# Kernel optimization log

Hardware: AMD Instinct MI355X
Metric: run time of the kernel (lower is better)

## Reference

```python
import jax, jax.numpy as jnp
import numpy as np

N_BLOCKS = 16
BLOCK_SIZE = 512
TOP_K = N_BLOCKS // 4  # matches n_blocks // 4 in the source


def setup_inputs() -> dict:
    key = jax.random.key(0)
    k1, k2, k3, k4, k5 = jax.random.split(key, 5)
    in_f, out_f = 2048, 8192
    x = jax.random.normal(k1, (2, 4096, in_f), dtype=jnp.float32)
    # router: Linear(in_features, n_blocks)
    Wr = jax.random.normal(k2, (N_BLOCKS, in_f), dtype=jnp.float32) * (in_f ** -0.5)
    br = jnp.zeros((N_BLOCKS,), dtype=jnp.float32)
    # fc1: Linear(in, out); fc2: Linear(out, in). Biases are unused in the original forward.
    W1 = jax.random.normal(k3, (out_f, in_f), dtype=jnp.float32) * (in_f ** -0.5)
    W2 = jax.random.normal(k4, (in_f, out_f), dtype=jnp.float32) * (out_f ** -0.5)
    return {"x": x, "Wr": Wr, "br": br, "W1": W1, "W2": W2}


def reference(x, Wr, br, W1, W2):
    x_shape = x.shape
    in_f = x_shape[-1]
    xf = x.reshape(-1, in_f)                      # [N, in]
    n = xf.shape[0]
    # router + top-k block selection per token
    prob = jax.nn.softmax(xf @ Wr.T + br, axis=-1)          # [N, nb]
    _, idx = jax.lax.top_k(prob, TOP_K)                      # [N, k]
    mask = jnp.zeros((n, N_BLOCKS), dtype=xf.dtype)
    mask = mask.at[jnp.arange(n)[:, None], idx].set(1.0)     # [N, nb]
    # fc1 per block: h[n,i,b] = x @ W1_block_i^T  (bias never used in source)
    W1b = W1.reshape(N_BLOCKS, BLOCK_SIZE, in_f)
    h = jnp.einsum('nf,ibf->nib', xf, W1b)                   # [N, nb, bs]
    # activation, then zero out unselected blocks (unselected never reach fc2)
    h = jax.nn.gelu(h, approximate=False) * mask[:, :, None]
    # fc2 per block accumulate: y = sum_i h_i @ W2_block_i^T
    W2b = W2.reshape(in_f, N_BLOCKS, BLOCK_SIZE)
    y = jnp.einsum('nib,fib->nf', h, W2b)                    # [N, in]
    return y.reshape(x_shape)
```

## Files before the change

kernel.cpp:

```cpp
#include <hip/hip_runtime.h>
#include <hip/hip_bf16.h>

#define N_TOK 8192
#define IN_F  2048
#define OUT_F 8192
#define NB    16
#define BS    512
#define BM    128
#define MAX_MT 272

typedef short          bf16x8  __attribute__((ext_vector_type(8)));
typedef unsigned short ushort8 __attribute__((ext_vector_type(8)));
typedef float          f32x4   __attribute__((ext_vector_type(4)));
typedef _Float16       f16x8   __attribute__((ext_vector_type(8)));

#define WS_COUNTS 0
#define WS_TSTART 64
#define WS_SEL    256
#define WS_INV    (32*1024)
#define WS_LISTS  (192*1024)
#define WS_XBF    (1ull<<20)
#define WS_W1BF   (WS_XBF + 33554432ull)
#define WS_W2BF   WS_XBF
#define WS_H      (WS_XBF + 67108864ull)
#define WS_YP     (WS_H + 35651584ull)

static __device__ __forceinline__ unsigned short f2bf(float f) {
    __hip_bfloat16 h = __float2bfloat16(f);
    return *reinterpret_cast<unsigned short*>(&h);
}

static __device__ __forceinline__ void gload16(const unsigned short* g, unsigned short* lds) {
    __builtin_amdgcn_global_load_lds(
        (const __attribute__((address_space(1))) unsigned int*)g,
        (__attribute__((address_space(3))) unsigned int*)lds, 16, 0, 0);
}

#define MFMA16(ai, bi) \
    acc[0][0] = __builtin_amdgcn_mfma_f32_16x16x32_bf16(ai##0, bi##0, acc[0][0], 0, 0, 0); \
    acc[0][1] = __builtin_amdgcn_mfma_f32_16x16x32_bf16(ai##0, bi##1, acc[0][1], 0, 0, 0); \
    acc[0][2] = __builtin_amdgcn_mfma_f32_16x16x32_bf16(ai##0, bi##2, acc[0][2], 0, 0, 0); \
    acc[0][3] = __builtin_amdgcn_mfma_f32_16x16x32_bf16(ai##0, bi##3, acc[0][3], 0, 0, 0); \
    acc[1][0] = __builtin_amdgcn_mfma_f32_16x16x32_bf16(ai##1, bi##0, acc[1][0], 0, 0, 0); \
    acc[1][1] = __builtin_amdgcn_mfma_f32_16x16x32_bf16(ai##1, bi##1, acc[1][1], 0, 0, 0); \
    acc[1][2] = __builtin_amdgcn_mfma_f32_16x16x32_bf16(ai##1, bi##2, acc[1][2], 0, 0, 0); \
    acc[1][3] = __builtin_amdgcn_mfma_f32_16x16x32_bf16(ai##1, bi##3, acc[1][3], 0, 0, 0); \
    acc[2][0] = __builtin_amdgcn_mfma_f32_16x16x32_bf16(ai##2, bi##0, acc[2][0], 0, 0, 0); \
    acc[2][1] = __builtin_amdgcn_mfma_f32_16x16x32_bf16(ai##2, bi##1, acc[2][1], 0, 0, 0); \
    acc[2][2] = __builtin_amdgcn_mfma_f32_16x16x32_bf16(ai##2, bi##2, acc[2][2], 0, 0, 0); \
    acc[2][3] = __builtin_amdgcn_mfma_f32_16x16x32_bf16(ai##2, bi##3, acc[2][3], 0, 0, 0); \
    acc[3][0] = __builtin_amdgcn_mfma_f32_16x16x32_bf16(ai##3, bi##0, acc[3][0], 0, 0, 0); \
    acc[3][1] = __builtin_amdgcn_mfma_f32_16x16x32_bf16(ai##3, bi##1, acc[3][1], 0, 0, 0); \
    acc[3][2] = __builtin_amdgcn_mfma_f32_16x16x32_bf16(ai##3, bi##2, acc[3][2], 0, 0, 0); \
    acc[3][3] = __builtin_amdgcn_mfma_f32_16x16x32_bf16(ai##3, bi##3, acc[3][3], 0, 0, 0);

__global__ __launch_bounds__(256) void router_kernel(
    const float* __restrict__ x, const float* __restrict__ Wr,
    const float* __restrict__ br, unsigned short* __restrict__ sel)
{
    const int tid = threadIdx.x;
    const int lt = tid & 63;
    const int wv = tid >> 6;
    const int tok = blockIdx.x * 4 + wv;
    const int e = lt >> 2, p = lt & 3;
    const float4* xp = (const float4*)(x + (size_t)tok * IN_F);
    const float4* wp = (const float4*)(Wr + (size_t)e * IN_F);
    double s = 0.0;
    for (int j = p; j < IN_F / 4; j += 4) {
        float4 a = xp[j], w = wp[j];
        s += (double)a.x * w.x + (double)a.y * w.y + (double)a.z * w.z + (double)a.w * w.w;
    }
    s += __shfl_down(s, 2);
    s += __shfl_down(s, 1);
    __shared__ double logits[4][NB];
    if (p == 0) logits[wv][e] = s + (double)br[e];
    __syncthreads();
    if (lt == 0) {
        unsigned used = 0, packed = 0;
        #pragma unroll
        for (int kk = 0; kk < 4; ++kk) {
            int best = 0; double bv = -1.0e300;
            #pragma unroll
            for (int i = 0; i < NB; ++i)
                if (!((used >> i) & 1u) && logits[wv][i] > bv) { bv = logits[wv][i]; best = i; }
            used |= 1u << best;
            packed |= (unsigned)best << (4 * kk);
        }
        sel[tok] = (unsigned short)packed;
    }
}

__global__ __launch_bounds__(256) void build_lists_kernel(
    const unsigned short* __restrict__ sel, int* __restrict__ counts,
    int* __restrict__ lists, unsigned* __restrict__ inv)
{
    const int e = blockIdx.x;
    const int t = threadIdx.x;
    unsigned short mysel[N_TOK / 256];
    int cnt = 0;
    #pragma unroll
    for (int i = 0; i < N_TOK / 256; ++i) {
        unsigned s = sel[i * 256 + t];
        mysel[i] = (unsigned short)s;
        bool m = ((s & 15u) == (unsigned)e) | (((s >> 4) & 15u) == (unsigned)e) |
                 (((s >> 8) & 15u) == (unsigned)e) | (((s >> 12) & 15u) == (unsigned)e);
        cnt += m ? 1 : 0;
    }
    __shared__ int ps[256];
    ps[t] = cnt;
    __syncthreads();
    #pragma unroll
    for (int off = 1; off < 256; off <<= 1) {
        int v = (t >= off) ? ps[t - off] : 0;
        __syncthreads();
        ps[t] += v;
        __syncthreads();
    }
    int pos = ps[t] - cnt;
    if (t == 255) counts[e] = ps[255];
    #pragma unroll
    for (int i = 0; i < N_TOK / 256; ++i) {
        unsigned s = mysel[i];
        bool m = ((s & 15u) == (unsigned)e) | (((s >> 4) & 15u) == (unsigned)e) |
                 (((s >> 8) & 15u) == (unsigned)e) | (((s >> 12) & 15u) == (unsigned)e);
        if (m) {
            const int tok = i * 256 + t;
            int j = ((s & 15u) == (unsigned)e) ? 0 :
                    (((s >> 4) & 15u) == (unsigned)e) ? 1 :
                    (((s >> 8) & 15u) == (unsigned)e) ? 2 : 3;
            inv[tok * 4 + j] = ((unsigned)e << 16) | (unsigned)pos;
            lists[e * N_TOK + pos++] = tok;
        }
    }
}

__global__ void scan_kernel(const int* __restrict__ counts, int* __restrict__ tstart)
{
    if (threadIdx.x == 0) {
        int acc = 0;
        for (int i = 0; i < NB; ++i) { tstart[i] = acc; acc += (counts[i] + BM - 1) / BM; }
        tstart[NB] = acc;
    }
}

__global__ __launch_bounds__(256) void convert_swz_kernel(
    const float* __restrict__ src, unsigned short* __restrict__ dst, int sh)
{
    const int total = 1 << 21;
    for (int id = blockIdx.x * 256 + threadIdx.x; id < total; id += 2048 * 256) {
        const int row = id >> sh;
        const int sr  = id & ((1 << sh) - 1);
        const int ps  = sr ^ (row & 7);
        const float4* s4 = (const float4*)(src + ((size_t)id << 3));
        float4 p0 = s4[0], p1 = s4[1];
        ushort8 o;
        o[0] = f2bf(p0.x); o[1] = f2bf(p0.y); o[2] = f2bf(p0.z); o[3] = f2bf(p0.w);
        o[4] = f2bf(p1.x); o[5] = f2bf(p1.y); o[6] = f2bf(p1.z); o[7] = f2bf(p1.w);
        *(ushort8*)(dst + (((size_t)(row) << sh) << 3) + ((size_t)ps << 3)) = o;
    }
}

__global__ __launch_bounds__(256) void fc1_kernel(
    const unsigned short* __restrict__ x_bf, const unsigned short* __restrict__ w1_bf,
    const int* __restrict__ lists, const int* __restrict__ counts,
    const int* __restrict__ tstart, unsigned short* __restrict__ h)
{
    __shared__ unsigned short As[2][BM * 64];
    __shared__ unsigned short Bs[2][BM * 64];
    const int bid = blockIdx.x;
    const int newid = (bid & 7) * 136 + (bid >> 3);
    const int nt = newid & 3, mt = newid >> 2;
    if (mt >= tstart[NB]) return;
    int b = 0;
    #pragma unroll
    for (int i = 1; i < NB; ++i) b += (mt >= tstart[i]);
    const int cnt  = counts[b];
    const int row0 = (mt - tstart[b]) * BM;
    const int tid  = threadIdx.x;
    const int wave = tid >> 6, lane = tid & 63;
    const int sr8 = lane >> 3, sph = lane & 7;

    const unsigned short* aS[4];
    const unsigned short* bS[4];
    const int loff = wave * 2048;
    #pragma unroll
    for (int t = 0; t < 4; ++t) {
        const int r = wave * 32 + t * 8 + sr8;
        const int gr = min(row0 + r, cnt - 1);
        const int tok = lists[b * N_TOK + gr];
        aS[t] = x_bf + (size_t)tok * IN_F + ((sph ^ sr8 ^ (tok & 7)) << 3);
        bS[t] = w1_bf + (size_t)(b * BS + nt * BM + r) * IN_F + (sph << 3);
    }

    const int lr16 = lane & 15, q = lane >> 4;
    const int wm = (wave >> 1) * 64, wn = (wave & 1) * 64;
    int offA[4], offB[4];
    #pragma unroll
    for (int i = 0; i < 4; ++i) {
        const int r = wm + i * 16 + lr16;
        offA[i] = r * 64 + ((q ^ (r & 7)) << 3);
    }
    #pragma unroll
    for (int j = 0; j < 4; ++j) {
        const int r = wn + j * 16 + lr16;
        offB[j] = r * 64 + ((q ^ (r & 7)) << 3);
    }

    f32x4 acc[4][4];
    #pragma unroll
    for (int i = 0; i < 4; ++i)
        #pragma unroll
        for (int j = 0; j < 4; ++j) acc[i][j] = (f32x4)0.0f;

    #pragma unroll
    for (int t = 0; t < 4; ++t) {
        gload16(aS[t], &As[0][loff + t * 512]);
        gload16(bS[t], &Bs[0][loff + t * 512]);
    }

    const int NK = IN_F / 64;
    for (int k = 0; k < NK; ++k) {
        const int cur = k & 1;
        if (k + 1 < NK) {
            const int ko = (k + 1) * 64;
            #pragma unroll
            for (int t = 0; t < 4; ++t) {
                gload16(aS[t] + ko, &As[cur ^ 1][loff + t * 512]);
                gload16(bS[t] + ko, &Bs[cur ^ 1][loff + t * 512]);
            }
            asm volatile("s_waitcnt vmcnt(8)" ::: "memory");
        } else {
            asm volatile("s_waitcnt vmcnt(0)" ::: "memory");
        }
        __builtin_amdgcn_s_barrier();
        __builtin_amdgcn_sched_barrier(0);
        {
            bf16x8 a0, a1, a2, a3, b0, b1, b2, b3;
            #pragma unroll
            for (int kk = 0; kk < 2; ++kk) {
                const int kx = kk << 5;
                a0 = *(const bf16x8*)&As[cur][offA[0] ^ kx];
                a1 = *(const bf16x8*)&As[cur][offA[1] ^ kx];
                a2 = *(const bf16x8*)&As[cur][offA[2] ^ kx];
                a3 = *(const bf16x8*)&As[cur][offA[3] ^ kx];
                b0 = *(const bf16x8*)&Bs[cur][offB[0] ^ kx];
                b1 = *(const bf16x8*)&Bs[cur][offB[1] ^ kx];
                b2 = *(const bf16x8*)&Bs[cur][offB[2] ^ kx];
                b3 = *(const bf16x8*)&Bs[cur][offB[3] ^ kx];
                __builtin_amdgcn_s_setprio(1);
                MFMA16(a, b)
                __builtin_amdgcn_s_setprio(0);
            }
        }
        __builtin_amdgcn_sched_barrier(0);
        __builtin_amdgcn_s_barrier();
    }
    #pragma unroll
    for (int i = 0; i < 4; ++i) {
        #pragma unroll
        for (int r = 0; r < 4; ++r) {
            const int lrow = wm + i * 16 + q * 4 + r;
            if (row0 + lrow < cnt) {
                const size_t hrow = (size_t)(mt * BM + lrow) * BS;
                const int r7 = (lrow & 7) << 3;
                #pragma unroll
                for (int j = 0; j < 4; ++j) {
                    const int col = nt * BM + wn + j * 16 + lr16;
                    float v = acc[i][j][r];
                    v = 0.5f * v * (1.0f + erff(v * 0.70710678118654752f));
                    h[hrow + (col ^ r7)] = f2bf(v);
                }
            }
        }
    }
}

__global__ __launch_bounds__(256) void fc2_kernel(
    const unsigned short* __restrict__ h, const unsigned short* __restrict__ w2_bf,
    const int* __restrict__ counts, const int* __restrict__ tstart,
    _Float16* __restrict__ yp)
{
    __shared__ unsigned short As[2][BM * 64];
    __shared__ unsigned short Bs[2][BM * 64];
    const int bid = blockIdx.x;
    const int newid = (bid & 7) * 544 + (bid >> 3);
    const int nt = newid & 15, mt = newid >> 4;
    if (mt >= tstart[NB]) return;
    int b = 0;
    #pragma unroll
    for (int i = 1; i < NB; ++i) b += (mt >= tstart[i]);
    const int cnt  = counts[b];
    const int row0 = (mt - tstart[b]) * BM;
    const int tid  = threadIdx.x;
    const int wave = tid >> 6, lane = tid & 63;
    const int sr8 = lane >> 3, sph = lane & 7;

    const unsigned short* aS[4];
    const unsigned short* bS[4];
    const int loff = wave * 2048;
    #pragma unroll
    for (int t = 0; t < 4; ++t) {
        const int r = wave * 32 + t * 8 + sr8;
        aS[t] = h + (size_t)(mt * BM + r) * BS + (sph << 3);
        bS[t] = w2_bf + (size_t)(nt * BM + r) * OUT_F + b * BS + (sph << 3);
    }

    const int lr16 = lane & 15, q = lane >> 4;
    const int wm = (wave >> 1) * 64, wn = (wave & 1) * 64;
    int offA[4], offB[4];
    #pragma unroll
    for (int i = 0; i < 4; ++i) {
        const int r = wm + i * 16 + lr16;
        offA[i] = r * 64 + ((q ^ (r & 7)) << 3);
    }
    #pragma unroll
    for (int j = 0; j < 4; ++j) {
        const int r = wn + j * 16 + lr16;
        offB[j] = r * 64 + ((q ^ (r & 7)) << 3);
    }

    f32x4 acc[4][4];
    #pragma unroll
    for (int i = 0; i < 4; ++i)
        #pragma unroll
        for (int j = 0; j < 4; ++j) acc[i][j] = (f32x4)0.0f;

    #pragma unroll
    for (int t = 0; t < 4; ++t) {
        gload16(aS[t], &As[0][loff + t * 512]);
        gload16(bS[t], &Bs[0][loff + t * 512]);
    }

    const int NK = BS / 64;
    for (int k = 0; k < NK; ++k) {
        const int cur = k & 1;
        if (k + 1 < NK) {
            const int ko = (k + 1) * 64;
            #pragma unroll
            for (int t = 0; t < 4; ++t) {
                gload16(aS[t] + ko, &As[cur ^ 1][loff + t * 512]);
                gload16(bS[t] + ko, &Bs[cur ^ 1][loff + t * 512]);
            }
            asm volatile("s_waitcnt vmcnt(8)" ::: "memory");
        } else {
            asm volatile("s_waitcnt vmcnt(0)" ::: "memory");
        }
        __builtin_amdgcn_s_barrier();
        __builtin_amdgcn_sched_barrier(0);
        {
            bf16x8 a0, a1, a2, a3, b0, b1, b2, b3;
            #pragma unroll
            for (int kk = 0; kk < 2; ++kk) {
                const int kx = kk << 5;
                a0 = *(const bf16x8*)&As[cur][offA[0] ^ kx];
                a1 = *(const bf16x8*)&As[cur][offA[1] ^ kx];
                a2 = *(const bf16x8*)&As[cur][offA[2] ^ kx];
                a3 = *(const bf16x8*)&As[cur][offA[3] ^ kx];
                b0 = *(const bf16x8*)&Bs[cur][offB[0] ^ kx];
                b1 = *(const bf16x8*)&Bs[cur][offB[1] ^ kx];
                b2 = *(const bf16x8*)&Bs[cur][offB[2] ^ kx];
                b3 = *(const bf16x8*)&Bs[cur][offB[3] ^ kx];
                __builtin_amdgcn_s_setprio(1);
                MFMA16(a, b)
                __builtin_amdgcn_s_setprio(0);
            }
        }
        __builtin_amdgcn_sched_barrier(0);
        __builtin_amdgcn_s_barrier();
    }
    #pragma unroll
    for (int i = 0; i < 4; ++i) {
        #pragma unroll
        for (int r = 0; r < 4; ++r) {
            const int lrow = wm + i * 16 + q * 4 + r;
            if (row0 + lrow < cnt) {
                _Float16* yrow = yp + (size_t)(mt * BM + lrow) * IN_F + nt * BM + wn + lr16;
                #pragma unroll
                for (int j = 0; j < 4; ++j)
                    yrow[j * 16] = (_Float16)acc[i][j][r];
            }
        }
    }
}

__global__ __launch_bounds__(256) void reduce_kernel(
    const _Float16* __restrict__ yp, const unsigned* __restrict__ inv,
    const int* __restrict__ tstart, float* __restrict__ y)
{
    const int tok = blockIdx.x;
    __shared__ size_t rbase[4];
    if (threadIdx.x < 4) {
        unsigned v = inv[tok * 4 + threadIdx.x];
        rbase[threadIdx.x] = (size_t)(tstart[v >> 16] * BM + (int)(v & 0xFFFFu)) * IN_F;
    }
    __syncthreads();
    const int c = threadIdx.x * 8;
    f16x8 v0 = *(const f16x8*)(yp + rbase[0] + c);
    f16x8 v1 = *(const f16x8*)(yp + rbase[1] + c);
    f16x8 v2 = *(const f16x8*)(yp + rbase[2] + c);
    f16x8 v3 = *(const f16x8*)(yp + rbase[3] + c);
    float out[8];
    #pragma unroll
    for (int j = 0; j < 8; ++j)
        out[j] = (float)v0[j] + (float)v1[j] + (float)v2[j] + (float)v3[j];
    float4* yo = (float4*)(y + (size_t)tok * IN_F + c);
    yo[0] = make_float4(out[0], out[1], out[2], out[3]);
    yo[1] = make_float4(out[4], out[5], out[6], out[7]);
}

extern "C" void kernel_launch(void* const* d_in, const int* in_sizes, int n_in,
                              void* d_out, int out_size, void* d_ws, size_t ws_size,
                              hipStream_t stream) {
    const float* x  = (const float*)d_in[0];
    const float* Wr = (const float*)d_in[1];
    const float* br = (const float*)d_in[2];
    const float* W1 = (const float*)d_in[3];
    const float* W2 = (const float*)d_in[4];
    float* y = (float*)d_out;
    char* ws = (char*)d_ws;
    int* counts = (int*)(ws + WS_COUNTS);
    int* tstart = (int*)(ws + WS_TSTART);
    unsigned short* sel = (unsigned short*)(ws + WS_SEL);
    unsigned* inv = (unsigned*)(ws + WS_INV);
    int* lists  = (int*)(ws + WS_LISTS);
    unsigned short* x_bf  = (unsigned short*)(ws + WS_XBF);
    unsigned short* w1_bf = (unsigned short*)(ws + WS_W1BF);
    unsigned short* w2_bf = (unsigned short*)(ws + WS_W2BF);
    unsigned short* h     = (unsigned short*)(ws + WS_H);
    _Float16* yp          = (_Float16*)(ws + WS_YP);

    hipLaunchKernelGGL(router_kernel, dim3(N_TOK / 4), dim3(256), 0, stream, x, Wr, br, sel);
    hipLaunchKernelGGL(build_lists_kernel, dim3(NB), dim3(256), 0, stream, sel, counts, lists, inv);
    hipLaunchKernelGGL(scan_kernel, dim3(1), dim3(64), 0, stream, counts, tstart);
    hipLaunchKernelGGL(convert_swz_kernel, dim3(2048), dim3(256), 0, stream, x,  x_bf,  8);
    hipLaunchKernelGGL(convert_swz_kernel, dim3(2048), dim3(256), 0, stream, W1, w1_bf, 8);
    hipLaunchKernelGGL(fc1_kernel, dim3(4 * MAX_MT), dim3(256), 0, stream, x_bf, w1_bf, lists, counts, tstart, h);
    hipLaunchKernelGGL(convert_swz_kernel, dim3(2048), dim3(256), 0, stream, W2, w2_bf, 10);
    hipLaunchKernelGGL(fc2_kernel, dim3(16 * MAX_MT), dim3(256), 0, stream, h, w2_bf, counts, tstart, yp);
    hipLaunchKernelGGL(reduce_kernel, dim3(N_TOK), dim3(256), 0, stream, yp, inv, tstart, y);
}
```

Baseline: 430.4 us.

## Enlarge expert GEMM tiles to 256 rows with 8 waves and triple-buffered LDS

```diff
diff --git a/kernel.cpp b/kernel.cpp
--- a/kernel.cpp
+++ b/kernel.cpp
@@ -6,8 +6,8 @@
 #define OUT_F 8192
 #define NB    16
 #define BS    512
-#define BM    128
-#define MAX_MT 272
+#define BM2   256
+#define MAX_MT2 144
 
 typedef short          bf16x8  __attribute__((ext_vector_type(8)));
 typedef unsigned short ushort8 __attribute__((ext_vector_type(8)));
@@ -20,10 +20,10 @@
 #define WS_INV    (32*1024)
 #define WS_LISTS  (192*1024)
 #define WS_XBF    (1ull<<20)
-#define WS_W1BF   (WS_XBF + 33554432ull)
 #define WS_W2BF   WS_XBF
-#define WS_H      (WS_XBF + 67108864ull)
-#define WS_YP     (WS_H + 35651584ull)
+#define WS_H      (WS_XBF + 33554432ull)
+#define WS_W1BF   (WS_H + 37748736ull)
+#define WS_YP     WS_W1BF
 
 static __device__ __forceinline__ unsigned short f2bf(float f) {
     __hip_bfloat16 h = __float2bfloat16(f);
@@ -54,6 +54,16 @@
     acc[3][2] = __builtin_amdgcn_mfma_f32_16x16x32_bf16(ai##3, bi##2, acc[3][2], 0, 0, 0); \
     acc[3][3] = __builtin_amdgcn_mfma_f32_16x16x32_bf16(ai##3, bi##3, acc[3][3], 0, 0, 0);
 
+#define PHASE_TAIL \
+    __builtin_amdgcn_s_barrier(); \
+    asm volatile("s_waitcnt lgkmcnt(0)" ::: "memory"); \
+    __builtin_amdgcn_sched_barrier(0); \
+    __builtin_amdgcn_s_setprio(1); \
+    MFMA16(a, b) \
+    __builtin_amdgcn_s_setprio(0); \
+    __builtin_amdgcn_sched_barrier(0); \
+    __builtin_amdgcn_s_barrier();
+
 __global__ __launch_bounds__(256) void router_kernel(
     const float* __restrict__ x, const float* __restrict__ Wr,
     const float* __restrict__ br, unsigned short* __restrict__ sel)
@@ -138,7 +148,7 @@
 {
     if (threadIdx.x == 0) {
         int acc = 0;
-        for (int i = 0; i < NB; ++i) { tstart[i] = acc; acc += (counts[i] + BM - 1) / BM; }
+        for (int i = 0; i < NB; ++i) { tstart[i] = acc; acc += (counts[i] + BM2 - 1) / BM2; }
         tstart[NB] = acc;
     }
 }
@@ -160,51 +170,49 @@
     }
 }
 
-__global__ __launch_bounds__(256) void fc1_kernel(
+__global__ __launch_bounds__(512) void fc1_kernel(
     const unsigned short* __restrict__ x_bf, const unsigned short* __restrict__ w1_bf,
     const int* __restrict__ lists, const int* __restrict__ counts,
     const int* __restrict__ tstart, unsigned short* __restrict__ h)
 {
-    __shared__ unsigned short As[2][BM * 64];
-    __shared__ unsigned short Bs[2][BM * 64];
+    __shared__ unsigned short lds[73728];
     const int bid = blockIdx.x;
-    const int newid = (bid & 7) * 136 + (bid >> 3);
+    const int newid = (bid & 7) * 72 + (bid >> 3);
     const int nt = newid & 3, mt = newid >> 2;
     if (mt >= tstart[NB]) return;
     int b = 0;
     #pragma unroll
     for (int i = 1; i < NB; ++i) b += (mt >= tstart[i]);
     const int cnt  = counts[b];
-    const int row0 = (mt - tstart[b]) * BM;
+    const int row0 = (mt - tstart[b]) * BM2;
     const int tid  = threadIdx.x;
     const int wave = tid >> 6, lane = tid & 63;
-    const int sr8 = lane >> 3, sph = lane & 7;
+    const int sph = lane & 7;
+    const int rbase = wave * 8 + (lane >> 3);
 
     const unsigned short* aS[4];
-    const unsigned short* bS[4];
-    const int loff = wave * 2048;
-    #pragma unroll
-    for (int t = 0; t < 4; ++t) {
-        const int r = wave * 32 + t * 8 + sr8;
+    const unsigned short* bS[2];
+    #pragma unroll
+    for (int i = 0; i < 4; ++i) {
+        const int r = i * 64 + rbase;
         const int gr = min(row0 + r, cnt - 1);
         const int tok = lists[b * N_TOK + gr];
-        aS[t] = x_bf + (size_t)tok * IN_F + ((sph ^ sr8 ^ (tok & 7)) << 3);
-        bS[t] = w1_bf + (size_t)(b * BS + nt * BM + r) * IN_F + (sph << 3);
-    }
+        aS[i] = x_bf + (size_t)tok * IN_F + ((sph ^ (r & 7) ^ (tok & 7)) << 3);
+    }
+    #pragma unroll
+    for (int j = 0; j < 2; ++j) {
+        const int r = j * 64 + rbase;
+        bS[j] = w1_bf + (size_t)(b * BS + nt * 128 + r) * IN_F + (sph << 3);
+    }
+    const int wbase = wave * 512;
 
     const int lr16 = lane & 15, q = lane >> 4;
     const int wm = (wave >> 1) * 64, wn = (wave & 1) * 64;
     int offA[4], offB[4];
     #pragma unroll
-    for (int i = 0; i < 4; ++i) {
-        const int r = wm + i * 16 + lr16;
-        offA[i] = r * 64 + ((q ^ (r & 7)) << 3);
-    }
-    #pragma unroll
-    for (int j = 0; j < 4; ++j) {
-        const int r = wn + j * 16 + lr16;
-        offB[j] = r * 64 + ((q ^ (r & 7)) << 3);
-    }
+    for (int i = 0; i < 4; ++i) { const int r = wm + i * 16 + lr16; offA[i] = r * 64 + ((q ^ (r & 7)) << 3); }
+    #pragma unroll
+    for (int j = 0; j < 4; ++j) { const int r = wn + j * 16 + lr16; offB[j] = r * 64 + ((q ^ (r & 7)) << 3); }
 
     f32x4 acc[4][4];
     #pragma unroll
@@ -212,48 +220,46 @@
         #pragma unroll
         for (int j = 0; j < 4; ++j) acc[i][j] = (f32x4)0.0f;
 
-    #pragma unroll
-    for (int t = 0; t < 4; ++t) {
-        gload16(aS[t], &As[0][loff + t * 512]);
-        gload16(bS[t], &Bs[0][loff + t * 512]);
-    }
+#define STA1(k, buf, i) gload16(aS[i] + (size_t)(k) * 64, lds + (buf) * 24576 + (i) * 4096 + wbase)
+#define STB1(k, buf, j) gload16(bS[j] + (size_t)(k) * 64, lds + (buf) * 24576 + 16384 + (j) * 4096 + wbase)
+
+    STA1(0,0,0); STA1(0,0,1); STA1(0,0,2); STA1(0,0,3); STB1(0,0,0); STB1(0,0,1);
+    STA1(1,1,0); STA1(1,1,1); STA1(1,1,2); STA1(1,1,3); STB1(1,1,0); STB1(1,1,1);
+    asm volatile("s_waitcnt vmcnt(6)" ::: "memory");
+    __builtin_amdgcn_s_barrier();
 
     const int NK = IN_F / 64;
+    int cur = 0;
     for (int k = 0; k < NK; ++k) {
-        const int cur = k & 1;
-        if (k + 1 < NK) {
-            const int ko = (k + 1) * 64;
-            #pragma unroll
-            for (int t = 0; t < 4; ++t) {
-                gload16(aS[t] + ko, &As[cur ^ 1][loff + t * 512]);
-                gload16(bS[t] + ko, &Bs[cur ^ 1][loff + t * 512]);
-            }
-            asm volatile("s_waitcnt vmcnt(8)" ::: "memory");
-        } else {
+        const unsigned short* Ab = lds + cur * 24576;
+        const unsigned short* Bb = Ab + 16384;
+        const int nxt = (cur == 0) ? 2 : cur - 1;
+        bf16x8 a0 = *(const bf16x8*)&Ab[offA[0]];
+        bf16x8 a1 = *(const bf16x8*)&Ab[offA[1]];
+        bf16x8 a2 = *(const bf16x8*)&Ab[offA[2]];
+        bf16x8 a3 = *(const bf16x8*)&Ab[offA[3]];
+        bf16x8 b0 = *(const bf16x8*)&Bb[offB[0]];
+        bf16x8 b1 = *(const bf16x8*)&Bb[offB[1]];
+        bf16x8 b2 = *(const bf16x8*)&Bb[offB[2]];
+        bf16x8 b3 = *(const bf16x8*)&Bb[offB[3]];
+        if (k + 2 < NK) { STA1(k + 2, nxt, 0); STA1(k + 2, nxt, 1); STB1(k + 2, nxt, 0); }
+        PHASE_TAIL
+        a0 = *(const bf16x8*)&Ab[offA[0] ^ 32];
+        a1 = *(const bf16x8*)&Ab[offA[1] ^ 32];
+        a2 = *(const bf16x8*)&Ab[offA[2] ^ 32];
+        a3 = *(const bf16x8*)&Ab[offA[3] ^ 32];
+        b0 = *(const bf16x8*)&Bb[offB[0] ^ 32];
+        b1 = *(const bf16x8*)&Bb[offB[1] ^ 32];
+        b2 = *(const bf16x8*)&Bb[offB[2] ^ 32];
+        b3 = *(const bf16x8*)&Bb[offB[3] ^ 32];
+        if (k + 2 < NK) {
+            STA1(k + 2, nxt, 2); STA1(k + 2, nxt, 3); STB1(k + 2, nxt, 1);
+            asm volatile("s_waitcnt vmcnt(6)" ::: "memory");
+        } else if (k + 1 < NK) {
             asm volatile("s_waitcnt vmcnt(0)" ::: "memory");
         }
-        __builtin_amdgcn_s_barrier();
-        __builtin_amdgcn_sched_barrier(0);
-        {
-            bf16x8 a0, a1, a2, a3, b0, b1, b2, b3;
-            #pragma unroll
-            for (int kk = 0; kk < 2; ++kk) {
-                const int kx = kk << 5;
-                a0 = *(const bf16x8*)&As[cur][offA[0] ^ kx];
-                a1 = *(const bf16x8*)&As[cur][offA[1] ^ kx];
-                a2 = *(const bf16x8*)&As[cur][offA[2] ^ kx];
-                a3 = *(const bf16x8*)&As[cur][offA[3] ^ kx];
-                b0 = *(const bf16x8*)&Bs[cur][offB[0] ^ kx];
-                b1 = *(const bf16x8*)&Bs[cur][offB[1] ^ kx];
-                b2 = *(const bf16x8*)&Bs[cur][offB[2] ^ kx];
-                b3 = *(const bf16x8*)&Bs[cur][offB[3] ^ kx];
-                __builtin_amdgcn_s_setprio(1);
-                MFMA16(a, b)
-                __builtin_amdgcn_s_setprio(0);
-            }
-        }
-        __builtin_amdgcn_sched_barrier(0);
-        __builtin_amdgcn_s_barrier();
+        PHASE_TAIL
+        cur = (cur == 2) ? 0 : cur + 1;
     }
     #pragma unroll
     for (int i = 0; i < 4; ++i) {
@@ -261,11 +267,11 @@
         for (int r = 0; r < 4; ++r) {
             const int lrow = wm + i * 16 + q * 4 + r;
             if (row0 + lrow < cnt) {
-                const size_t hrow = (size_t)(mt * BM + lrow) * BS;
+                const size_t hrow = (size_t)(mt * BM2 + lrow) * BS;
                 const int r7 = (lrow & 7) << 3;
                 #pragma unroll
                 for (int j = 0; j < 4; ++j) {
-                    const int col = nt * BM + wn + j * 16 + lr16;
+                    const int col = nt * 128 + wn + j * 16 + lr16;
                     float v = acc[i][j][r];
                     v = 0.5f * v * (1.0f + erff(v * 0.70710678118654752f));
                     h[hrow + (col ^ r7)] = f2bf(v);
@@ -273,51 +279,51 @@
             }
         }
     }
-}
-
-__global__ __launch_bounds__(256) void fc2_kernel(
+#undef STA1
+#undef STB1
+}
+
+__global__ __launch_bounds__(512) void fc2_kernel(
     const unsigned short* __restrict__ h, const unsigned short* __restrict__ w2_bf,
     const int* __restrict__ counts, const int* __restrict__ tstart,
     _Float16* __restrict__ yp)
 {
-    __shared__ unsigned short As[2][BM * 64];
-    __shared__ unsigned short Bs[2][BM * 64];
+    __shared__ unsigned short lds[73728];
     const int bid = blockIdx.x;
-    const int newid = (bid & 7) * 544 + (bid >> 3);
+    const int newid = (bid & 7) * 288 + (bid >> 3);
     const int nt = newid & 15, mt = newid >> 4;
     if (mt >= tstart[NB]) return;
     int b = 0;
     #pragma unroll
     for (int i = 1; i < NB; ++i) b += (mt >= tstart[i]);
     const int cnt  = counts[b];
-    const int row0 = (mt - tstart[b]) * BM;
+    const int row0 = (mt - tstart[b]) * BM2;
     const int tid  = threadIdx.x;
     const int wave = tid >> 6, lane = tid & 63;
-    const int sr8 = lane >> 3, sph = lane & 7;
+    const int sph = lane & 7;
+    const int rbase = wave * 8 + (lane >> 3);
 
     const unsigned short* aS[4];
-    const unsigned short* bS[4];
-    const int loff = wave * 2048;
-    #pragma unroll
-    for (int t = 0; t < 4; ++t) {
-        const int r = wave * 32 + t * 8 + sr8;
-        aS[t] = h + (size_t)(mt * BM + r) * BS + (sph << 3);
-        bS[t] = w2_bf + (size_t)(nt * BM + r) * OUT_F + b * BS + (sph << 3);
-    }
+    const unsigned short* bS[2];
+    #pragma unroll
+    for (int i = 0; i < 4; ++i) {
+        const int r = i * 64 + rbase;
+        aS[i] = h + (size_t)(mt * BM2 + r) * BS + (sph << 3);
+    }
+    #pragma unroll
+    for (int j = 0; j < 2; ++j) {
+        const int r = j * 64 + rbase;
+        bS[j] = w2_bf + (size_t)(nt * 128 + r) * OUT_F + b * BS + (sph << 3);
+    }
+    const int wbase = wave * 512;
 
     const int lr16 = lane & 15, q = lane >> 4;
     const int wm = (wave >> 1) * 64, wn = (wave & 1) * 64;
     int offA[4], offB[4];
     #pragma unroll
-    for (int i = 0; i < 4; ++i) {
-        const int r = wm + i * 16 + lr16;
-        offA[i] = r * 64 + ((q ^ (r & 7)) << 3);
-    }
-    #pragma unroll
-    for (int j = 0; j < 4; ++j) {
-        const int r = wn + j * 16 + lr16;
-        offB[j] = r * 64 + ((q ^ (r & 7)) << 3);
-    }
+    for (int i = 0; i < 4; ++i) { const int r = wm + i * 16 + lr16; offA[i] = r * 64 + ((q ^ (r & 7)) << 3); }
+    #pragma unroll
+    for (int j = 0; j < 4; ++j) { const int r = wn + j * 16 + lr16; offB[j] = r * 64 + ((q ^ (r & 7)) << 3); }
 
     f32x4 acc[4][4];
     #pragma unroll
@@ -325,48 +331,46 @@
         #pragma unroll
         for (int j = 0; j < 4; ++j) acc[i][j] = (f32x4)0.0f;
 
-    #pragma unroll
-    for (int t = 0; t < 4; ++t) {
-        gload16(aS[t], &As[0][loff + t * 512]);
-        gload16(bS[t], &Bs[0][loff + t * 512]);
-    }
+#define STA2(k, buf, i) gload16(aS[i] + (size_t)(k) * 64, lds + (buf) * 24576 + (i) * 4096 + wbase)
+#define STB2(k, buf, j) gload16(bS[j] + (size_t)(k) * 64, lds + (buf) * 24576 + 16384 + (j) * 4096 + wbase)
+
+    STA2(0,0,0); STA2(0,0,1); STA2(0,0,2); STA2(0,0,3); STB2(0,0,0); STB2(0,0,1);
+    STA2(1,1,0); STA2(1,1,1); STA2(1,1,2); STA2(1,1,3); STB2(1,1,0); STB2(1,1,1);
+    asm volatile("s_waitcnt vmcnt(6)" ::: "memory");
+    __builtin_amdgcn_s_barrier();
 
     const int NK = BS / 64;
+    int cur = 0;
     for (int k = 0; k < NK; ++k) {
-        const int cur = k & 1;
-        if (k + 1 < NK) {
-            const int ko = (k + 1) * 64;
-            #pragma unroll
-            for (int t = 0; t < 4; ++t) {
-                gload16(aS[t] + ko, &As[cur ^ 1][loff + t * 512]);
-                gload16(bS[t] + ko, &Bs[cur ^ 1][loff + t * 512]);
-            }
-            asm volatile("s_waitcnt vmcnt(8)" ::: "memory");
-        } else {
+        const unsigned short* Ab = lds + cur * 24576;
+        const unsigned short* Bb = Ab + 16384;
+        const int nxt = (cur == 0) ? 2 : cur - 1;
+        bf16x8 a0 = *(const bf16x8*)&Ab[offA[0]];
+        bf16x8 a1 = *(const bf16x8*)&Ab[offA[1]];
+        bf16x8 a2 = *(const bf16x8*)&Ab[offA[2]];
+        bf16x8 a3 = *(const bf16x8*)&Ab[offA[3]];
+        bf16x8 b0 = *(const bf16x8*)&Bb[offB[0]];
+        bf16x8 b1 = *(const bf16x8*)&Bb[offB[1]];
+        bf16x8 b2 = *(const bf16x8*)&Bb[offB[2]];
+        bf16x8 b3 = *(const bf16x8*)&Bb[offB[3]];
+        if (k + 2 < NK) { STA2(k + 2, nxt, 0); STA2(k + 2, nxt, 1); STB2(k + 2, nxt, 0); }
+        PHASE_TAIL
+        a0 = *(const bf16x8*)&Ab[offA[0] ^ 32];
+        a1 = *(const bf16x8*)&Ab[offA[1] ^ 32];
+        a2 = *(const bf16x8*)&Ab[offA[2] ^ 32];
+        a3 = *(const bf16x8*)&Ab[offA[3] ^ 32];
+        b0 = *(const bf16x8*)&Bb[offB[0] ^ 32];
+        b1 = *(const bf16x8*)&Bb[offB[1] ^ 32];
+        b2 = *(const bf16x8*)&Bb[offB[2] ^ 32];
+        b3 = *(const bf16x8*)&Bb[offB[3] ^ 32];
+        if (k + 2 < NK) {
+            STA2(k + 2, nxt, 2); STA2(k + 2, nxt, 3); STB2(k + 2, nxt, 1);
+            asm volatile("s_waitcnt vmcnt(6)" ::: "memory");
+        } else if (k + 1 < NK) {
             asm volatile("s_waitcnt vmcnt(0)" ::: "memory");
         }
-        __builtin_amdgcn_s_barrier();
-        __builtin_amdgcn_sched_barrier(0);
-        {
-            bf16x8 a0, a1, a2, a3, b0, b1, b2, b3;
-            #pragma unroll
-            for (int kk = 0; kk < 2; ++kk) {
-                const int kx = kk << 5;
-                a0 = *(const bf16x8*)&As[cur][offA[0] ^ kx];
-                a1 = *(const bf16x8*)&As[cur][offA[1] ^ kx];
-                a2 = *(const bf16x8*)&As[cur][offA[2] ^ kx];
-                a3 = *(const bf16x8*)&As[cur][offA[3] ^ kx];
-                b0 = *(const bf16x8*)&Bs[cur][offB[0] ^ kx];
-                b1 = *(const bf16x8*)&Bs[cur][offB[1] ^ kx];
-                b2 = *(const bf16x8*)&Bs[cur][offB[2] ^ kx];
-                b3 = *(const bf16x8*)&Bs[cur][offB[3] ^ kx];
-                __builtin_amdgcn_s_setprio(1);
-                MFMA16(a, b)
-                __builtin_amdgcn_s_setprio(0);
-            }
-        }
-        __builtin_amdgcn_sched_barrier(0);
-        __builtin_amdgcn_s_barrier();
+        PHASE_TAIL
+        cur = (cur == 2) ? 0 : cur + 1;
     }
     #pragma unroll
     for (int i = 0; i < 4; ++i) {
@@ -374,13 +378,15 @@
         for (int r = 0; r < 4; ++r) {
             const int lrow = wm + i * 16 + q * 4 + r;
             if (row0 + lrow < cnt) {
-                _Float16* yrow = yp + (size_t)(mt * BM + lrow) * IN_F + nt * BM + wn + lr16;
+                _Float16* yrow = yp + (size_t)(mt * BM2 + lrow) * IN_F + nt * 128 + wn + lr16;
                 #pragma unroll
                 for (int j = 0; j < 4; ++j)
                     yrow[j * 16] = (_Float16)acc[i][j][r];
             }
         }
     }
+#undef STA2
+#undef STB2
 }
 
 __global__ __launch_bounds__(256) void reduce_kernel(
@@ -391,7 +397,7 @@
     __shared__ size_t rbase[4];
     if (threadIdx.x < 4) {
         unsigned v = inv[tok * 4 + threadIdx.x];
-        rbase[threadIdx.x] = (size_t)(tstart[v >> 16] * BM + (int)(v & 0xFFFFu)) * IN_F;
+        rbase[threadIdx.x] = (size_t)(tstart[v >> 16] * BM2 + (int)(v & 0xFFFFu)) * IN_F;
     }
     __syncthreads();
     const int c = threadIdx.x * 8;
@@ -434,8 +440,8 @@
     hipLaunchKernelGGL(scan_kernel, dim3(1), dim3(64), 0, stream, counts, tstart);
     hipLaunchKernelGGL(convert_swz_kernel, dim3(2048), dim3(256), 0, stream, x,  x_bf,  8);
     hipLaunchKernelGGL(convert_swz_kernel, dim3(2048), dim3(256), 0, stream, W1, w1_bf, 8);
-    hipLaunchKernelGGL(fc1_kernel, dim3(4 * MAX_MT), dim3(256), 0, stream, x_bf, w1_bf, lists, counts, tstart, h);
+    hipLaunchKernelGGL(fc1_kernel, dim3(4 * MAX_MT2), dim3(512), 0, stream, x_bf, w1_bf, lists, counts, tstart, h);
     hipLaunchKernelGGL(convert_swz_kernel, dim3(2048), dim3(256), 0, stream, W2, w2_bf, 10);
-    hipLaunchKernelGGL(fc2_kernel, dim3(16 * MAX_MT), dim3(256), 0, stream, h, w2_bf, counts, tstart, yp);
+    hipLaunchKernelGGL(fc2_kernel, dim3(16 * MAX_MT2), dim3(512), 0, stream, h, w2_bf, counts, tstart, yp);
     hipLaunchKernelGGL(reduce_kernel, dim3(N_TOK), dim3(256), 0, stream, yp, inv, tstart, y);
 }
```

Result: faster. 407.5 us (-5.3%).

## Gather routed tokens into contiguous padded bf16 buffer before fc1

Applied to the files above, without the earlier changes.

```diff
diff --git a/kernel.cpp b/kernel.cpp
--- a/kernel.cpp
+++ b/kernel.cpp
@@ -19,11 +19,11 @@
 #define WS_SEL    256
 #define WS_INV    (32*1024)
 #define WS_LISTS  (192*1024)
-#define WS_XBF    (1ull<<20)
-#define WS_W1BF   (WS_XBF + 33554432ull)
-#define WS_W2BF   WS_XBF
-#define WS_H      (WS_XBF + 67108864ull)
-#define WS_YP     (WS_H + 35651584ull)
+#define WS_XG     (1ull<<20)
+#define WS_YP     WS_XG
+#define WS_H      (WS_XG + 142606336ull)
+#define WS_W1BF   (WS_H + 35651584ull)
+#define WS_W2BF   WS_W1BF
 
 static __device__ __forceinline__ unsigned short f2bf(float f) {
     __hip_bfloat16 h = __float2bfloat16(f);
@@ -143,7 +143,7 @@
     }
 }
 
-__global__ __launch_bounds__(256) void convert_swz_kernel(
+__global__ __launch_bounds__(256) void convert_w_kernel(
     const float* __restrict__ src, unsigned short* __restrict__ dst, int sh)
 {
     const int total = 1 << 21;
@@ -160,9 +160,36 @@
     }
 }
 
+__global__ __launch_bounds__(256) void convert_gather_kernel(
+    const float* __restrict__ x, const int* __restrict__ lists,
+    const int* __restrict__ counts, const int* __restrict__ tstart,
+    unsigned short* __restrict__ xg)
+{
+    const int row = blockIdx.x;
+    const int mt = row >> 7;
+    if (mt >= tstart[NB]) return;
+    int b = 0;
+    #pragma unroll
+    for (int i = 1; i < NB; ++i) b += (mt >= tstart[i]);
+    const int pos = row - tstart[b] * BM;
+    const int t = threadIdx.x;
+    unsigned short* drow = xg + (size_t)row * IN_F;
+    if (pos < counts[b]) {
+        const int tok = lists[b * N_TOK + pos];
+        const float4* s4 = (const float4*)(x + (size_t)tok * IN_F + t * 8);
+        float4 p0 = s4[0], p1 = s4[1];
+        ushort8 o;
+        o[0] = f2bf(p0.x); o[1] = f2bf(p0.y); o[2] = f2bf(p0.z); o[3] = f2bf(p0.w);
+        o[4] = f2bf(p1.x); o[5] = f2bf(p1.y); o[6] = f2bf(p1.z); o[7] = f2bf(p1.w);
+        *(ushort8*)(drow + ((t ^ (row & 7)) << 3)) = o;
+    } else {
+        *(ushort8*)(drow + (t << 3)) = (ushort8)0;
+    }
+}
+
+
 __global__ __launch_bounds__(256) void fc1_kernel(
-    const unsigned short* __restrict__ x_bf, const unsigned short* __restrict__ w1_bf,
-    const int* __restrict__ lists, const int* __restrict__ counts,
+    const unsigned short* __restrict__ xg, const unsigned short* __restrict__ w1_bf,
     const int* __restrict__ tstart, unsigned short* __restrict__ h)
 {
     __shared__ unsigned short As[2][BM * 64];
@@ -174,8 +201,6 @@
     int b = 0;
     #pragma unroll
     for (int i = 1; i < NB; ++i) b += (mt >= tstart[i]);
-    const int cnt  = counts[b];
-    const int row0 = (mt - tstart[b]) * BM;
     const int tid  = threadIdx.x;
     const int wave = tid >> 6, lane = tid & 63;
     const int sr8 = lane >> 3, sph = lane & 7;
@@ -186,9 +211,7 @@
     #pragma unroll
     for (int t = 0; t < 4; ++t) {
         const int r = wave * 32 + t * 8 + sr8;
-        const int gr = min(row0 + r, cnt - 1);
-        const int tok = lists[b * N_TOK + gr];
-        aS[t] = x_bf + (size_t)tok * IN_F + ((sph ^ sr8 ^ (tok & 7)) << 3);
+        aS[t] = xg + (size_t)(mt * BM + r) * IN_F + (sph << 3);
         bS[t] = w1_bf + (size_t)(b * BS + nt * BM + r) * IN_F + (sph << 3);
     }
 
@@ -196,15 +219,9 @@
     const int wm = (wave >> 1) * 64, wn = (wave & 1) * 64;
     int offA[4], offB[4];
     #pragma unroll
-    for (int i = 0; i < 4; ++i) {
-        const int r = wm + i * 16 + lr16;
-        offA[i] = r * 64 + ((q ^ (r & 7)) << 3);
-    }
-    #pragma unroll
-    for (int j = 0; j < 4; ++j) {
-        const int r = wn + j * 16 + lr16;
-        offB[j] = r * 64 + ((q ^ (r & 7)) << 3);
-    }
+    for (int i = 0; i < 4; ++i) { const int r = wm + i * 16 + lr16; offA[i] = r * 64 + ((q ^ (r & 7)) << 3); }
+    #pragma unroll
+    for (int j = 0; j < 4; ++j) { const int r = wn + j * 16 + lr16; offB[j] = r * 64 + ((q ^ (r & 7)) << 3); }
 
     f32x4 acc[4][4];
     #pragma unroll
@@ -260,16 +277,14 @@
         #pragma unroll
         for (int r = 0; r < 4; ++r) {
             const int lrow = wm + i * 16 + q * 4 + r;
-            if (row0 + lrow < cnt) {
-                const size_t hrow = (size_t)(mt * BM + lrow) * BS;
-                const int r7 = (lrow & 7) << 3;
-                #pragma unroll
-                for (int j = 0; j < 4; ++j) {
-                    const int col = nt * BM + wn + j * 16 + lr16;
-                    float v = acc[i][j][r];
-                    v = 0.5f * v * (1.0f + erff(v * 0.70710678118654752f));
-                    h[hrow + (col ^ r7)] = f2bf(v);
-                }
+            const size_t hrow = (size_t)(mt * BM + lrow) * BS;
+            const int r7 = (lrow & 7) << 3;
+            #pragma unroll
+            for (int j = 0; j < 4; ++j) {
+                const int col = nt * BM + wn + j * 16 + lr16;
+                float v = acc[i][j][r];
+                v = 0.5f * v * (1.0f + erff(v * 0.70710678118654752f));
+                h[hrow + (col ^ r7)] = f2bf(v);
             }
         }
     }
@@ -277,8 +292,7 @@
 
 __global__ __launch_bounds__(256) void fc2_kernel(
     const unsigned short* __restrict__ h, const unsigned short* __restrict__ w2_bf,
-    const int* __restrict__ counts, const int* __restrict__ tstart,
-    _Float16* __restrict__ yp)
+    const int* __restrict__ tstart, _Float16* __restrict__ yp)
 {
     __shared__ unsigned short As[2][BM * 64];
     __shared__ unsigned short Bs[2][BM * 64];
@@ -289,8 +303,6 @@
     int b = 0;
     #pragma unroll
     for (int i = 1; i < NB; ++i) b += (mt >= tstart[i]);
-    const int cnt  = counts[b];
-    const int row0 = (mt - tstart[b]) * BM;
     const int tid  = threadIdx.x;
     const int wave = tid >> 6, lane = tid & 63;
     const int sr8 = lane >> 3, sph = lane & 7;
@@ -309,15 +321,9 @@
     const int wm = (wave >> 1) * 64, wn = (wave & 1) * 64;
     int offA[4], offB[4];
     #pragma unroll
-    for (int i = 0; i < 4; ++i) {
-        const int r = wm + i * 16 + lr16;
-        offA[i] = r * 64 + ((q ^ (r & 7)) << 3);
-    }
-    #pragma unroll
-    for (int j = 0; j < 4; ++j) {
-        const int r = wn + j * 16 + lr16;
-        offB[j] = r * 64 + ((q ^ (r & 7)) << 3);
-    }
+    for (int i = 0; i < 4; ++i) { const int r = wm + i * 16 + lr16; offA[i] = r * 64 + ((q ^ (r & 7)) << 3); }
+    #pragma unroll
+    for (int j = 0; j < 4; ++j) { const int r = wn + j * 16 + lr16; offB[j] = r * 64 + ((q ^ (r & 7)) << 3); }
 
     f32x4 acc[4][4];
     #pragma unroll
@@ -373,12 +379,10 @@
         #pragma unroll
         for (int r = 0; r < 4; ++r) {
             const int lrow = wm + i * 16 + q * 4 + r;
-            if (row0 + lrow < cnt) {
-                _Float16* yrow = yp + (size_t)(mt * BM + lrow) * IN_F + nt * BM + wn + lr16;
-                #pragma unroll
-                for (int j = 0; j < 4; ++j)
-                    yrow[j * 16] = (_Float16)acc[i][j][r];
-            }
+            _Float16* yrow = yp + (size_t)(mt * BM + lrow) * IN_F + nt * BM + wn + lr16;
+            #pragma unroll
+            for (int j = 0; j < 4; ++j)
+                yrow[j * 16] = (_Float16)acc[i][j][r];
         }
     }
 }
@@ -423,7 +427,7 @@
     unsigned short* sel = (unsigned short*)(ws + WS_SEL);
     unsigned* inv = (unsigned*)(ws + WS_INV);
     int* lists  = (int*)(ws + WS_LISTS);
-    unsigned short* x_bf  = (unsigned short*)(ws + WS_XBF);
+    unsigned short* xg    = (unsigned short*)(ws + WS_XG);
     unsigned short* w1_bf = (unsigned short*)(ws + WS_W1BF);
     unsigned short* w2_bf = (unsigned short*)(ws + WS_W2BF);
     unsigned short* h     = (unsigned short*)(ws + WS_H);
@@ -432,10 +436,10 @@
     hipLaunchKernelGGL(router_kernel, dim3(N_TOK / 4), dim3(256), 0, stream, x, Wr, br, sel);
     hipLaunchKernelGGL(build_lists_kernel, dim3(NB), dim3(256), 0, stream, sel, counts, lists, inv);
     hipLaunchKernelGGL(scan_kernel, dim3(1), dim3(64), 0, stream, counts, tstart);
-    hipLaunchKernelGGL(convert_swz_kernel, dim3(2048), dim3(256), 0, stream, x,  x_bf,  8);
-    hipLaunchKernelGGL(convert_swz_kernel, dim3(2048), dim3(256), 0, stream, W1, w1_bf, 8);
-    hipLaunchKernelGGL(fc1_kernel, dim3(4 * MAX_MT), dim3(256), 0, stream, x_bf, w1_bf, lists, counts, tstart, h);
-    hipLaunchKernelGGL(convert_swz_kernel, dim3(2048), dim3(256), 0, stream, W2, w2_bf, 10);
-    hipLaunchKernelGGL(fc2_kernel, dim3(16 * MAX_MT), dim3(256), 0, stream, h, w2_bf, counts, tstart, yp);
+    hipLaunchKernelGGL(convert_w_kernel, dim3(2048), dim3(256), 0, stream, W1, w1_bf, 8);
+    hipLaunchKernelGGL(convert_gather_kernel, dim3(MAX_MT * BM), dim3(256), 0, stream, x, lists, counts, tstart, xg);
+    hipLaunchKernelGGL(fc1_kernel, dim3(4 * MAX_MT), dim3(256), 0, stream, xg, w1_bf, tstart, h);
+    hipLaunchKernelGGL(convert_w_kernel, dim3(2048), dim3(256), 0, stream, W2, w2_bf, 10);
+    hipLaunchKernelGGL(fc2_kernel, dim3(16 * MAX_MT), dim3(256), 0, stream, h, w2_bf, tstart, yp);
     hipLaunchKernelGGL(reduce_kernel, dim3(N_TOK), dim3(256), 0, stream, yp, inv, tstart, y);
 }
```

Result: slower. 505.5 us (+17.5%).
